# Kernel tuning notes

Measured on AMD Instinct MI355X. Metric: run time of the kernel, lower is better.

Reference implementation:

```python
import jax, jax.numpy as jnp
import numpy as np

TAU = 1.0
EPS = 1e-10
LN_EPS = 1e-5

def _layernorm(x, g, b):
    m = jnp.mean(x, axis=-1, keepdims=True)
    v = jnp.mean((x - m) ** 2, axis=-1, keepdims=True)
    return (x - m) * jax.lax.rsqrt(v + LN_EPS) * g + b

def setup_inputs() -> dict:
    key = jax.random.key(0)
    N, D = 12288, 128
    ks = jax.random.split(key, 12)
    s = 1.0 / np.sqrt(D)
    inp = {
        "x": jax.random.normal(ks[0], (N, D), jnp.float32),
        "adj": jax.random.uniform(ks[1], (N, N), jnp.float32),
        "u": jax.random.uniform(ks[2], (N, 2), jnp.float32),
        "W1": jax.random.normal(ks[3], (D, D), jnp.float32) * s,
        "b1": jnp.zeros((D,), jnp.float32),
        "W2": jax.random.normal(ks[4], (D, D), jnp.float32) * s,
        "b2": jnp.zeros((D,), jnp.float32),
        "Wg": jax.random.normal(ks[5], (2 * D, D), jnp.float32) * s,
        "bg": jnp.zeros((D,), jnp.float32),
        "Wn": jax.random.normal(ks[6], (D, 2), jnp.float32) * s,
        "bn": jnp.zeros((2,), jnp.float32),
        "g_in": jnp.ones((D,), jnp.float32),
        "b_in": jnp.zeros((D,), jnp.float32),
        "g_out": jnp.ones((D,), jnp.float32),
        "b_out": jnp.zeros((D,), jnp.float32),
    }
    return inp

def reference(x, adj, u, W1, b1, W2, b2, Wg, bg, Wn, bn, g_in, b_in, g_out, b_out):
    residual = x
    x_norm = _layernorm(x, g_in, b_in)                      # [N, D]
    logits = x_norm @ Wn + bn                                # [N, 2]
    gumbel = -jnp.log(-jnp.log(jnp.clip(u, EPS, 1.0)) + EPS)
    y_soft = jax.nn.softmax((logits + gumbel) / TAU, axis=-1)
    hard = jax.nn.one_hot(jnp.argmax(y_soft, axis=-1), 2, dtype=y_soft.dtype)
    y = hard + y_soft - jax.lax.stop_gradient(y_soft)        # straight-through
    gate = y[:, 1]                                           # [N]
    sel_adj = adj * gate[:, None] * gate[None, :]            # [N, N]
    view1 = x_norm
    view2 = sel_adj @ x_norm                                 # [N, D]
    fusion_gate = jax.nn.sigmoid(jnp.concatenate([view1, view2], axis=-1) @ Wg + bg)
    fused = fusion_gate * (view1 @ W1 + b1) + (1.0 - fusion_gate) * (view2 @ W2 + b2)
    return _layernorm(fused + residual, g_out, b_out)
```

## Files before the change

### kernel.cpp

```cpp
#include <hip/hip_runtime.h>

#define DD 128
#define KSPLIT 8
#define BM 64
#define BK 64
#define K3R 32

typedef float f4 __attribute__((ext_vector_type(4)));
typedef _Float16 h4 __attribute__((ext_vector_type(4)));
typedef _Float16 h8 __attribute__((ext_vector_type(8)));
typedef unsigned int u32x4 __attribute__((ext_vector_type(4)));

__global__ __launch_bounds__(256) void k1_ln_gate(
    const float* __restrict__ x, const float* __restrict__ u,
    const float* __restrict__ Wn, const float* __restrict__ bn,
    const float* __restrict__ g_in, const float* __restrict__ b_in,
    float* __restrict__ x_norm, float* __restrict__ gatef,
    int* __restrict__ rows_sel, int* __restrict__ cnt, int N) {
  int wave = threadIdx.x >> 6, lane = threadIdx.x & 63;
  int row = blockIdx.x * 4 + wave;
  if (row >= N) return;
  int d0 = lane, d1 = lane + 64;
  float x0 = x[(size_t)row * DD + d0];
  float x1 = x[(size_t)row * DD + d1];
  float s = x0 + x1;
#pragma unroll
  for (int off = 32; off; off >>= 1) s += __shfl_xor(s, off, 64);
  float mean = s * (1.0f / 128.0f);
  float dx0 = x0 - mean, dx1 = x1 - mean;
  float v = dx0 * dx0 + dx1 * dx1;
#pragma unroll
  for (int off = 32; off; off >>= 1) v += __shfl_xor(v, off, 64);
  float inv = 1.0f / sqrtf(v * (1.0f / 128.0f) + 1e-5f);
  float xn0 = dx0 * inv * g_in[d0] + b_in[d0];
  float xn1 = dx1 * inv * g_in[d1] + b_in[d1];
  x_norm[(size_t)row * DD + d0] = xn0;
  x_norm[(size_t)row * DD + d1] = xn1;
  float l0 = xn0 * Wn[2 * d0] + xn1 * Wn[2 * d1];
  float l1 = xn0 * Wn[2 * d0 + 1] + xn1 * Wn[2 * d1 + 1];
#pragma unroll
  for (int off = 32; off; off >>= 1) {
    l0 += __shfl_xor(l0, off, 64);
    l1 += __shfl_xor(l1, off, 64);
  }
  float u0 = u[2 * row], u1 = u[2 * row + 1];
  float g0 = -logf(-logf(fminf(fmaxf(u0, 1e-10f), 1.0f)) + 1e-10f);
  float g1 = -logf(-logf(fminf(fmaxf(u1, 1e-10f), 1.0f)) + 1e-10f);
  float z0 = l0 + bn[0] + g0;
  float z1 = l1 + bn[1] + g1;
  bool gate = (z1 > z0);
  if (lane == 0) {
    gatef[row] = gate ? 1.0f : 0.0f;
    if (gate) {
      int p = atomicAdd(cnt, 1);
      rows_sel[p] = row;
    }
  }
}

__global__ __launch_bounds__(256) void k1b_transpose(
    const float* __restrict__ x_norm, const float* __restrict__ gatef,
    _Float16* __restrict__ xg16T, int N) {
  __shared__ float tile[64][65];
  const int n0 = blockIdx.x * 64;
  const int d0 = blockIdx.y * 64;
  const int t = threadIdx.x;
  {
    const int c4 = (t & 15) * 4, r0 = t >> 4;
#pragma unroll
    for (int uu = 0; uu < 4; ++uu) {
      int r = r0 + 16 * uu;
      float gv = gatef[n0 + r];
      f4 v = *(const f4*)(x_norm + (size_t)(n0 + r) * DD + d0 + c4);
#pragma unroll
      for (int j = 0; j < 4; ++j) tile[r][c4 + j] = v[j] * gv;
    }
  }
  __syncthreads();
  {
    const int nq = t & 15, dr0 = t >> 4;
#pragma unroll
    for (int uu = 0; uu < 4; ++uu) {
      int d = dr0 + 16 * uu;
      h4 o;
#pragma unroll
      for (int j = 0; j < 4; ++j) o[j] = (_Float16)tile[nq * 4 + j][d];
      *(h4*)(xg16T + (size_t)(d0 + d) * N + n0 + nq * 4) = o;
    }
  }
}

__global__ __launch_bounds__(256) void k2_mfma(
    const float* __restrict__ adj, const _Float16* __restrict__ xg16T,
    const int* __restrict__ rows_sel, const int* __restrict__ cnt,
    float* __restrict__ view2p, int N) {
  __shared__ __align__(16) unsigned short Ab[BM * BK];
  __shared__ __align__(16) unsigned short Bb[DD * BK];
  __shared__ int rloc[BM];
  const int Nc = *cnt;
  const int rbase = blockIdx.x * BM;
  if (rbase >= Nc) return;
  const int t = threadIdx.x;
  if (t < BM) {
    int m = rbase + t;
    rloc[t] = rows_sel[m < Nc ? m : Nc - 1];
  }
  __syncthreads();
  const int lane = t & 63, wave = t >> 6;
  const int li = lane & 15, g = lane >> 4;
  const int am = t >> 2, asub = t & 3;
  const size_t arow = (size_t)rloc[am] * (size_t)N;
  const int aswz = (am & 7) << 4;
  const int bd = t >> 1, bhalf = t & 1;
  const size_t brow = (size_t)bd * (size_t)N;
  const int bswz = (bd & 7) << 4;
  const int arbyte = (wave * 16 + li) * (BK * 2);
  const int fswz = (li & 7) << 4;

  f4 acc[8];
#pragma unroll
  for (int i = 0; i < 8; ++i) acc[i] = (f4){0.f, 0.f, 0.f, 0.f};

  const int kchunk = N / KSPLIT;
  const int kbeg = blockIdx.y * kchunk;

  for (int kt = 0; kt < kchunk; kt += BK) {
    const int k0 = kbeg + kt;
    __syncthreads();
#pragma unroll
    for (int i = 0; i < 4; ++i) {
      int q = asub + 4 * i;
      f4 v = *(const f4*)(adj + arow + (size_t)(k0 + q * 4));
      h4 hv;
      hv[0] = (_Float16)v[0];
      hv[1] = (_Float16)v[1];
      hv[2] = (_Float16)v[2];
      hv[3] = (_Float16)v[3];
      *(h4*)((char*)Ab + am * (BK * 2) + ((q * 8) ^ aswz)) = hv;
    }
#pragma unroll
    for (int i = 0; i < 4; ++i) {
      int boff = bhalf * 64 + i * 16;
      u32x4 v = *(const u32x4*)((const char*)xg16T + (brow + (size_t)k0) * 2 + boff);
      *(u32x4*)((char*)Bb + bd * (BK * 2) + (boff ^ bswz)) = v;
    }
    __syncthreads();
#pragma unroll
    for (int s = 0; s < 2; ++s) {
      h8 af = *(const h8*)((const char*)Ab + arbyte + ((s * 64 + g * 16) ^ fswz));
#pragma unroll
      for (int c = 0; c < 8; ++c) {
        int br = c * 16 + li;
        h8 bf = *(const h8*)((const char*)Bb + br * (BK * 2) +
                             ((s * 64 + g * 16) ^ fswz));
        acc[c] = __builtin_amdgcn_mfma_f32_16x16x32_f16(af, bf, acc[c], 0, 0, 0);
      }
    }
  }
  const size_t plane = (size_t)blockIdx.y * (size_t)N * DD;
#pragma unroll
  for (int c = 0; c < 8; ++c) {
#pragma unroll
    for (int r = 0; r < 4; ++r) {
      int mi = wave * 16 + g * 4 + r;
      if (rbase + mi < Nc)
        view2p[plane + (size_t)rloc[mi] * DD + c * 16 + li] = acc[c][r];
    }
  }
}

__global__ __launch_bounds__(256) void k3_epilogue(
    const float* __restrict__ x, const float* __restrict__ x_norm,
    const float* __restrict__ view2p, const float* __restrict__ gatef,
    const float* __restrict__ W1, const float* __restrict__ b1,
    const float* __restrict__ W2, const float* __restrict__ b2,
    const float* __restrict__ Wg, const float* __restrict__ bg,
    const float* __restrict__ g_out, const float* __restrict__ b_out,
    float* __restrict__ out, int N) {
  __shared__ float t1[K3R][DD];
  __shared__ float t2[K3R][DD];
  const int row0 = blockIdx.x * K3R;
  const int t = threadIdx.x;
  {
    const int cs = (t & 31) * 4, rs = t >> 5;
#pragma unroll
    for (int uu = 0; uu < 4; ++uu) {
      int r = rs + 8 * uu;
      int row = row0 + r;
      *(f4*)&t1[r][cs] = *(const f4*)(x_norm + (size_t)row * DD + cs);
      f4 sum = {0.f, 0.f, 0.f, 0.f};
      if (gatef[row] != 0.0f) {
#pragma unroll
        for (int ks = 0; ks < KSPLIT; ++ks)
          sum += *(const f4*)(view2p + ((size_t)ks * N + row) * DD + cs);
      }
      *(f4*)&t2[r][cs] = sum;
    }
  }
  __syncthreads();
  const int rg = t >> 5;
  const int cb = (t & 31) * 4;
  f4 zero = {0.f, 0.f, 0.f, 0.f};
  f4 fg4[4] = {zero, zero, zero, zero};
  f4 h14[4] = {zero, zero, zero, zero};
  f4 h24[4] = {zero, zero, zero, zero};
#pragma unroll 2
  for (int j = 0; j < DD; ++j) {
    f4 wg1 = *(const f4*)(Wg + j * DD + cb);
    f4 wg2 = *(const f4*)(Wg + (j + DD) * DD + cb);
    f4 w1 = *(const f4*)(W1 + j * DD + cb);
    f4 w2 = *(const f4*)(W2 + j * DD + cb);
#pragma unroll
    for (int rr = 0; rr < 4; ++rr) {
      float tv1 = t1[rg * 4 + rr][j];
      float tv2 = t2[rg * 4 + rr][j];
      fg4[rr] += tv1 * wg1 + tv2 * wg2;
      h14[rr] += tv1 * w1;
      h24[rr] += tv2 * w2;
    }
  }
  f4 bgv = *(const f4*)(bg + cb);
  f4 b1v = *(const f4*)(b1 + cb);
  f4 b2v = *(const f4*)(b2 + cb);
  f4 goutv = *(const f4*)(g_out + cb);
  f4 boutv = *(const f4*)(b_out + cb);
#pragma unroll
  for (int rr = 0; rr < 4; ++rr) {
    int row = row0 + rg * 4 + rr;
    f4 fg;
#pragma unroll
    for (int c = 0; c < 4; ++c)
      fg[c] = 1.0f / (1.0f + expf(-(fg4[rr][c] + bgv[c])));
    f4 h1 = h14[rr] + b1v;
    f4 h2 = h24[rr] + b2v;
    f4 fused = fg * h1 + (1.0f - fg) * h2;
    f4 xres = *(const f4*)(x + (size_t)row * DD + cb);
    f4 sres = fused + xres;
    float ps = sres[0] + sres[1] + sres[2] + sres[3];
#pragma unroll
    for (int off = 16; off; off >>= 1) ps += __shfl_xor(ps, off, 32);
    float mean = ps * (1.0f / 128.0f);
    f4 dx = sres - mean;
    float pq = dx[0] * dx[0] + dx[1] * dx[1] + dx[2] * dx[2] + dx[3] * dx[3];
#pragma unroll
    for (int off = 16; off; off >>= 1) pq += __shfl_xor(pq, off, 32);
    float inv = 1.0f / sqrtf(pq * (1.0f / 128.0f) + 1e-5f);
    f4 o = dx * inv * goutv + boutv;
    *(f4*)(out + (size_t)row * DD + cb) = o;
  }
}

extern "C" void kernel_launch(void* const* d_in, const int* in_sizes, int n_in,
                              void* d_out, int out_size, void* d_ws, size_t ws_size,
                              hipStream_t stream) {
  const float* x = (const float*)d_in[0];
  const float* adj = (const float*)d_in[1];
  const float* u = (const float*)d_in[2];
  const float* W1 = (const float*)d_in[3];
  const float* b1 = (const float*)d_in[4];
  const float* W2 = (const float*)d_in[5];
  const float* b2 = (const float*)d_in[6];
  const float* Wg = (const float*)d_in[7];
  const float* bg = (const float*)d_in[8];
  const float* Wn = (const float*)d_in[9];
  const float* bn = (const float*)d_in[10];
  const float* g_in = (const float*)d_in[11];
  const float* b_in = (const float*)d_in[12];
  const float* g_out = (const float*)d_in[13];
  const float* b_out = (const float*)d_in[14];
  float* out = (float*)d_out;

  const int N = in_sizes[2] / 2;

  char* ws = (char*)d_ws;
  int* cnt = (int*)ws;
  int* rows_sel = (int*)(ws + 256);
  size_t o_gate = 256 + (size_t)N * 4;
  float* gatef = (float*)(ws + o_gate);
  size_t o_xn = o_gate + (size_t)N * 4;
  float* x_norm = (float*)(ws + o_xn);
  size_t o_xt = o_xn + (size_t)N * DD * 4;
  _Float16* xg16T = (_Float16*)(ws + o_xt);
  size_t o_v2p = o_xt + (size_t)DD * N * 2;
  float* view2p = (float*)(ws + o_v2p);

  hipMemsetAsync(cnt, 0, 4, stream);

  k1_ln_gate<<<N / 4, 256, 0, stream>>>(x, u, Wn, bn, g_in, b_in, x_norm, gatef,
                                        rows_sel, cnt, N);
  k1b_transpose<<<dim3(N / 64, DD / 64), 256, 0, stream>>>(x_norm, gatef, xg16T, N);
  k2_mfma<<<dim3(N / BM, KSPLIT), 256, 0, stream>>>(adj, xg16T, rows_sel, cnt,
                                                    view2p, N);
  k3_epilogue<<<N / K3R, 256, 0, stream>>>(x, x_norm, view2p, gatef, W1, b1, W2,
                                           b2, Wg, bg, g_out, b_out, out, N);
}
```

Baseline: 898.7 us.

## Enlarge k2 row tile, double K-split, and prefetch next tile into registers

Measured after the change: 897.6 us. About the same (-0.1%).

```diff
diff --git a/kernel.cpp b/kernel.cpp
--- a/kernel.cpp
+++ b/kernel.cpp
@@ -1,8 +1,8 @@
 #include <hip/hip_runtime.h>
 
 #define DD 128
-#define KSPLIT 8
-#define BM 64
+#define KSPLIT 16
+#define BM 128
 #define BK 64
 #define K3R 32
 
@@ -90,7 +90,7 @@
   }
 }
 
-__global__ __launch_bounds__(256) void k2_mfma(
+__global__ __launch_bounds__(256, 3) void k2_mfma(
     const float* __restrict__ adj, const _Float16* __restrict__ xg16T,
     const int* __restrict__ rows_sel, const int* __restrict__ cnt,
     float* __restrict__ view2p, int N) {
@@ -108,52 +108,73 @@
   __syncthreads();
   const int lane = t & 63, wave = t >> 6;
   const int li = lane & 15, g = lane >> 4;
-  const int am = t >> 2, asub = t & 3;
-  const size_t arow = (size_t)rloc[am] * (size_t)N;
-  const int aswz = (am & 7) << 4;
-  const int bd = t >> 1, bhalf = t & 1;
-  const size_t brow = (size_t)bd * (size_t)N;
-  const int bswz = (bd & 7) << 4;
-  const int arbyte = (wave * 16 + li) * (BK * 2);
+  const int srow = t >> 1, shalf = t & 1;
+  const size_t agbase = (size_t)rloc[srow] * (size_t)N + (size_t)(shalf * 32);
+  const size_t bgrow = (size_t)srow * (size_t)N;
+  const int sswz = (srow & 7) << 4;
   const int fswz = (li & 7) << 4;
 
-  f4 acc[8];
-#pragma unroll
-  for (int i = 0; i < 8; ++i) acc[i] = (f4){0.f, 0.f, 0.f, 0.f};
+  f4 acc0[8], acc1[8];
+#pragma unroll
+  for (int i = 0; i < 8; ++i) {
+    acc0[i] = (f4){0.f, 0.f, 0.f, 0.f};
+    acc1[i] = (f4){0.f, 0.f, 0.f, 0.f};
+  }
 
   const int kchunk = N / KSPLIT;
   const int kbeg = blockIdx.y * kchunk;
-
-  for (int kt = 0; kt < kchunk; kt += BK) {
-    const int k0 = kbeg + kt;
+  const int ntiles = kchunk / BK;
+
+  f4 areg[8];
+  u32x4 breg[4];
+  {
+    const float* ap = adj + agbase + kbeg;
+#pragma unroll
+    for (int j = 0; j < 8; ++j) areg[j] = *(const f4*)(ap + j * 4);
+    const char* bp = (const char*)xg16T + (bgrow + (size_t)kbeg) * 2 + shalf * 64;
+#pragma unroll
+    for (int i = 0; i < 4; ++i) breg[i] = *(const u32x4*)(bp + i * 16);
+  }
+
+  for (int kt = 0; kt < ntiles; ++kt) {
     __syncthreads();
-#pragma unroll
-    for (int i = 0; i < 4; ++i) {
-      int q = asub + 4 * i;
-      f4 v = *(const f4*)(adj + arow + (size_t)(k0 + q * 4));
-      h4 hv;
-      hv[0] = (_Float16)v[0];
-      hv[1] = (_Float16)v[1];
-      hv[2] = (_Float16)v[2];
-      hv[3] = (_Float16)v[3];
-      *(h4*)((char*)Ab + am * (BK * 2) + ((q * 8) ^ aswz)) = hv;
-    }
-#pragma unroll
-    for (int i = 0; i < 4; ++i) {
-      int boff = bhalf * 64 + i * 16;
-      u32x4 v = *(const u32x4*)((const char*)xg16T + (brow + (size_t)k0) * 2 + boff);
-      *(u32x4*)((char*)Bb + bd * (BK * 2) + (boff ^ bswz)) = v;
+    {
+      char* abase = (char*)Ab + srow * (BK * 2);
+#pragma unroll
+      for (int j2 = 0; j2 < 4; ++j2) {
+        f4 v0 = areg[2 * j2], v1 = areg[2 * j2 + 1];
+        h8 hv;
+        hv[0] = (_Float16)v0[0]; hv[1] = (_Float16)v0[1];
+        hv[2] = (_Float16)v0[2]; hv[3] = (_Float16)v0[3];
+        hv[4] = (_Float16)v1[0]; hv[5] = (_Float16)v1[1];
+        hv[6] = (_Float16)v1[2]; hv[7] = (_Float16)v1[3];
+        *(h8*)(abase + ((shalf * 64 + j2 * 16) ^ sswz)) = hv;
+      }
+      char* bbase = (char*)Bb + srow * (BK * 2);
+#pragma unroll
+      for (int i = 0; i < 4; ++i)
+        *(u32x4*)(bbase + ((shalf * 64 + i * 16) ^ sswz)) = breg[i];
     }
     __syncthreads();
+    if (kt + 1 < ntiles) {
+      const int k0 = kbeg + (kt + 1) * BK;
+      const float* ap = adj + agbase + k0;
+#pragma unroll
+      for (int j = 0; j < 8; ++j) areg[j] = *(const f4*)(ap + j * 4);
+      const char* bp = (const char*)xg16T + (bgrow + (size_t)k0) * 2 + shalf * 64;
+#pragma unroll
+      for (int i = 0; i < 4; ++i) breg[i] = *(const u32x4*)(bp + i * 16);
+    }
 #pragma unroll
     for (int s = 0; s < 2; ++s) {
-      h8 af = *(const h8*)((const char*)Ab + arbyte + ((s * 64 + g * 16) ^ fswz));
+      const int koff = (s * 64 + g * 16) ^ fswz;
+      h8 af0 = *(const h8*)((const char*)Ab + (wave * 32 + li) * (BK * 2) + koff);
+      h8 af1 = *(const h8*)((const char*)Ab + (wave * 32 + 16 + li) * (BK * 2) + koff);
 #pragma unroll
       for (int c = 0; c < 8; ++c) {
-        int br = c * 16 + li;
-        h8 bf = *(const h8*)((const char*)Bb + br * (BK * 2) +
-                             ((s * 64 + g * 16) ^ fswz));
-        acc[c] = __builtin_amdgcn_mfma_f32_16x16x32_f16(af, bf, acc[c], 0, 0, 0);
+        h8 bf = *(const h8*)((const char*)Bb + (c * 16 + li) * (BK * 2) + koff);
+        acc0[c] = __builtin_amdgcn_mfma_f32_16x16x32_f16(af0, bf, acc0[c], 0, 0, 0);
+        acc1[c] = __builtin_amdgcn_mfma_f32_16x16x32_f16(af1, bf, acc1[c], 0, 0, 0);
       }
     }
   }
@@ -161,10 +182,13 @@
 #pragma unroll
   for (int c = 0; c < 8; ++c) {
 #pragma unroll
-    for (int r = 0; r < 4; ++r) {
-      int mi = wave * 16 + g * 4 + r;
-      if (rbase + mi < Nc)
-        view2p[plane + (size_t)rloc[mi] * DD + c * 16 + li] = acc[c][r];
+    for (int q = 0; q < 4; ++q) {
+      int mi0 = wave * 32 + g * 4 + q;
+      int mi1 = mi0 + 16;
+      if (rbase + mi0 < Nc)
+        view2p[plane + (size_t)rloc[mi0] * DD + c * 16 + li] = acc0[c][q];
+      if (rbase + mi1 < Nc)
+        view2p[plane + (size_t)rloc[mi1] * DD + c * 16 + li] = acc1[c][q];
     }
   }
 }
```
